# Kernel optimization log

Hardware: AMD Instinct MI355X
Metric: run time of the kernel (lower is better)

## Reference

```python
import jax, jax.numpy as jnp
from jax import lax
import numpy as np

T, B, INPUT_SIZE, HIDDEN, LAYERS, OUT_DIM = 256, 1000, 300, 2, 2, 1


def setup_inputs() -> dict:
    key = jax.random.key(0)
    ks = jax.random.split(key, 12)
    H4 = 4 * HIDDEN
    s = 0.1
    return {
        "x": jax.random.normal(ks[0], (T, B, INPUT_SIZE), dtype=jnp.float32),
        "h0": jnp.zeros((LAYERS, B, HIDDEN), dtype=jnp.float32),
        "c0": jnp.zeros((LAYERS, B, HIDDEN), dtype=jnp.float32),
        "W_ih0": jax.random.normal(ks[1], (H4, INPUT_SIZE), dtype=jnp.float32) * s,
        "W_hh0": jax.random.normal(ks[2], (H4, HIDDEN), dtype=jnp.float32) * s,
        "b_ih0": jax.random.normal(ks[3], (H4,), dtype=jnp.float32) * s,
        "b_hh0": jax.random.normal(ks[4], (H4,), dtype=jnp.float32) * s,
        "W_ih1": jax.random.normal(ks[5], (H4, HIDDEN), dtype=jnp.float32) * s,
        "W_hh1": jax.random.normal(ks[6], (H4, HIDDEN), dtype=jnp.float32) * s,
        "b_ih1": jax.random.normal(ks[7], (H4,), dtype=jnp.float32) * s,
        "b_hh1": jax.random.normal(ks[8], (H4,), dtype=jnp.float32) * s,
        "W_lin": jax.random.normal(ks[9], (OUT_DIM, HIDDEN), dtype=jnp.float32) * s,
        "b_lin": jax.random.normal(ks[10], (OUT_DIM,), dtype=jnp.float32) * s,
    }


def _lstm_layer(x, h0, c0, W_ih, W_hh, b_ih, b_hh):
    # x: [T, B, D_in]; PyTorch gate order i, f, g, o.
    # Precompute input projections for all timesteps at once (one big GEMM).
    xg = jnp.einsum('tbd,gd->tbg', x, W_ih) + (b_ih + b_hh)  # [T, B, 4H]

    def step(carry, xt):
        h, c = carry
        gates = xt + h @ W_hh.T  # [B, 4H]
        i, f, g, o = jnp.split(gates, 4, axis=-1)
        c = jax.nn.sigmoid(f) * c + jax.nn.sigmoid(i) * jnp.tanh(g)
        h = jax.nn.sigmoid(o) * jnp.tanh(c)
        return (h, c), h

    (_, _), ys = lax.scan(step, (h0, c0), xg)
    return ys  # [T, B, H]


def reference(x, h0, c0, W_ih0, W_hh0, b_ih0, b_hh0, W_ih1, W_hh1, b_ih1, b_hh1, W_lin, b_lin):
    y0 = _lstm_layer(x, h0[0], c0[0], W_ih0, W_hh0, b_ih0, b_hh0)   # [T, B, H]
    y1 = _lstm_layer(y0, h0[1], c0[1], W_ih1, W_hh1, b_ih1, b_hh1)  # [T, B, H]
    pred = y1[-1] @ W_lin.T + b_lin  # [B, 1]
    return pred.reshape(-1)          # [B]
```

## Files before the change

kernel.cpp:

```cpp
#include <hip/hip_runtime.h>

#define T_STEPS 256
#define BATCH   1000
#define D_IN    300
#define H4      8
#define ROWS    32
#define TILE_F4 2400
#define NT      8
#define NBLK    1000

#define L2E   1.4426950408889634f
#define L2E2  2.8853900817779268f

__device__ __forceinline__ float fexp2(float x) {
#if __has_builtin(__builtin_amdgcn_exp2f)
    return __builtin_amdgcn_exp2f(x);
#else
    return exp2f(x);
#endif
}
__device__ __forceinline__ float sig2(float x) {
    return __builtin_amdgcn_rcpf(1.0f + fexp2(-x));
}
__device__ __forceinline__ float tanh2(float x) {
    return fmaf(-2.0f, __builtin_amdgcn_rcpf(1.0f + fexp2(x)), 1.0f);
}

__device__ __forceinline__ void gload16(const float4* g, float4* l) {
    __builtin_amdgcn_global_load_lds(
        (const __attribute__((address_space(1))) void*)g,
        (__attribute__((address_space(3))) void*)l, 16, 0, 0);
}

__global__ __launch_bounds__(256) void xproj_kernel(
    const float* __restrict__ x, const float* __restrict__ W,
    const float* __restrict__ b_ih, const float* __restrict__ b_hh,
    float* __restrict__ xg)
{
    __shared__ __align__(16) float xs[2][2560 * 4];
    __shared__ __align__(16) float ws[768 * 4];

    const int tid   = threadIdx.x;
    const int wbase = tid & ~63;

    const float4* xf4 = (const float4*)x;
    const float4* wf4 = (const float4*)W;
    float4* xs0 = (float4*)xs[0];
    float4* xs1 = (float4*)xs[1];
    float4* wsf = (float4*)ws;

    const long tile0 = (long)blockIdx.x * NT;

    const int g = tid & 7;
    const int r = tid >> 3;
    const float bias  = b_ih[g] + b_hh[g];
    const float scale = (g == 4 || g == 5) ? L2E2 : L2E;

#pragma unroll
    for (int j = 0; j < 3; ++j) {
        int k  = j * 256 + tid;
        int gk = k < 600 ? k : 599;
        gload16(wf4 + gk, wsf + (j * 256 + wbase));
    }
#pragma unroll
    for (int j = 0; j < 10; ++j) {
        int k  = j * 256 + tid;
        int gk = k < TILE_F4 ? k : TILE_F4 - 1;
        gload16(xf4 + tile0 * TILE_F4 + gk, xs0 + (j * 256 + wbase));
    }
    asm volatile("s_waitcnt vmcnt(0)" ::: "memory");
    __builtin_amdgcn_s_barrier();

    const float4* wr = wsf + g * 75;

    for (int i = 0; i < NT; ++i) {
        if (i + 1 < NT) {
            float4* nbuf = (i & 1) ? xs0 : xs1;
            long tb = (tile0 + i + 1) * TILE_F4;
#pragma unroll
            for (int j = 0; j < 10; ++j) {
                int k  = j * 256 + tid;
                int gk = k < TILE_F4 ? k : TILE_F4 - 1;
                gload16(xf4 + tb + gk, nbuf + (j * 256 + wbase));
            }
        }

        const float4* xr = ((i & 1) ? xs1 : xs0) + r * 75;
        float a0 = 0.f, a1 = 0.f, a2 = 0.f, a3 = 0.f;
#pragma unroll 5
        for (int k = 0; k < 75; ++k) {
            float4 xv = xr[k];
            float4 wv = wr[k];
            a0 += xv.x * wv.x; a1 += xv.y * wv.y;
            a2 += xv.z * wv.z; a3 += xv.w * wv.w;
        }
        xg[(tile0 + i) * 256 + tid] = ((a0 + a1) + (a2 + a3) + bias) * scale;

        if (i + 1 < NT) {
            asm volatile("s_waitcnt vmcnt(1)" ::: "memory");
            __builtin_amdgcn_s_barrier();
        }
    }
}

__global__ __launch_bounds__(64) void lstm_seq_kernel(
    const float* __restrict__ xg,
    const float* __restrict__ h0in, const float* __restrict__ c0in,
    const float* __restrict__ Whh0, const float* __restrict__ Wih1,
    const float* __restrict__ Whh1, const float* __restrict__ bih1,
    const float* __restrict__ bhh1, const float* __restrict__ Wlin,
    const float* __restrict__ blin, float* __restrict__ out)
{
    int b = blockIdx.x * 64 + threadIdx.x;
    bool active = (b < BATCH);
    int bb = active ? b : (BATCH - 1);

    float whh0[H4][2], wih1[H4][2], whh1[H4][2], bias1[H4];
#pragma unroll
    for (int k = 0; k < H4; ++k) {
        float f = (k == 4 || k == 5) ? L2E2 : L2E;
        whh0[k][0] = Whh0[2 * k] * f; whh0[k][1] = Whh0[2 * k + 1] * f;
        wih1[k][0] = Wih1[2 * k] * f; wih1[k][1] = Wih1[2 * k + 1] * f;
        whh1[k][0] = Whh1[2 * k] * f; whh1[k][1] = Whh1[2 * k + 1] * f;
        bias1[k]   = (bih1[k] + bhh1[k]) * f;
    }

    float h0a = h0in[2 * bb],             h0b = h0in[2 * bb + 1];
    float c0a = c0in[2 * bb],             c0b = c0in[2 * bb + 1];
    float h1a = h0in[2 * BATCH + 2 * bb], h1b = h0in[2 * BATCH + 2 * bb + 1];
    float c1a = c0in[2 * BATCH + 2 * bb], c1b = c0in[2 * BATCH + 2 * bb + 1];

    const float4* __restrict__ xp = (const float4*)xg;

    float4 plo[4], phi[4];
#pragma unroll
    for (int t = 0; t < 4; ++t) {
        plo[t] = xp[(t * BATCH + bb) * 2];
        phi[t] = xp[(t * BATCH + bb) * 2 + 1];
    }

    float p[H4];
#pragma unroll
    for (int k = 0; k < H4; ++k)
        p[k] = bias1[k] + h1a * whh1[k][0] + h1b * whh1[k][1];

#pragma unroll 4
    for (int t = 0; t < T_STEPS; ++t) {
        int s = t & 3;
        float4 l4 = plo[s], h4 = phi[s];
        if (t + 4 < T_STEPS) {
            plo[s] = xp[((t + 4) * BATCH + bb) * 2];
            phi[s] = xp[((t + 4) * BATCH + bb) * 2 + 1];
        }
        float xv[H4] = {l4.x, l4.y, l4.z, l4.w, h4.x, h4.y, h4.z, h4.w};

        float gt[H4];
#pragma unroll
        for (int k = 0; k < H4; ++k)
            gt[k] = xv[k] + h0a * whh0[k][0] + h0b * whh0[k][1];
        c0a = sig2(gt[2]) * c0a + sig2(gt[0]) * tanh2(gt[4]);
        c0b = sig2(gt[3]) * c0b + sig2(gt[1]) * tanh2(gt[5]);
        h0a = sig2(gt[6]) * tanh2(c0a * L2E2);
        h0b = sig2(gt[7]) * tanh2(c0b * L2E2);

        float qt[H4];
#pragma unroll
        for (int k = 0; k < H4; ++k)
            qt[k] = p[k] + h0a * wih1[k][0] + h0b * wih1[k][1];
        c1a = sig2(qt[2]) * c1a + sig2(qt[0]) * tanh2(qt[4]);
        c1b = sig2(qt[3]) * c1b + sig2(qt[1]) * tanh2(qt[5]);
        h1a = sig2(qt[6]) * tanh2(c1a * L2E2);
        h1b = sig2(qt[7]) * tanh2(c1b * L2E2);

#pragma unroll
        for (int k = 0; k < H4; ++k)
            p[k] = bias1[k] + h1a * whh1[k][0] + h1b * whh1[k][1];
    }

    if (active)
        out[b] = h1a * Wlin[0] + h1b * Wlin[1] + blin[0];
}

extern "C" void kernel_launch(void* const* d_in, const int* in_sizes, int n_in,
                              void* d_out, int out_size, void* d_ws, size_t ws_size,
                              hipStream_t stream) {
    const float* x      = (const float*)d_in[0];
    const float* h0     = (const float*)d_in[1];
    const float* c0     = (const float*)d_in[2];
    const float* W_ih0  = (const float*)d_in[3];
    const float* W_hh0  = (const float*)d_in[4];
    const float* b_ih0  = (const float*)d_in[5];
    const float* b_hh0  = (const float*)d_in[6];
    const float* W_ih1  = (const float*)d_in[7];
    const float* W_hh1  = (const float*)d_in[8];
    const float* b_ih1  = (const float*)d_in[9];
    const float* b_hh1  = (const float*)d_in[10];
    const float* W_lin  = (const float*)d_in[11];
    const float* b_lin  = (const float*)d_in[12];
    float* out = (float*)d_out;
    float* xg  = (float*)d_ws;

    xproj_kernel<<<NBLK, 256, 0, stream>>>(x, W_ih0, b_ih0, b_hh0, xg);
    lstm_seq_kernel<<<(BATCH + 63) / 64, 64, 0, stream>>>(
        xg, h0, c0, W_hh0, W_ih1, W_hh1, b_ih1, b_hh1, W_lin, b_lin, out);
}
```

Before: 588.5 us.

## Rewrite input projection to stream x directly with quad-lane split-K dot products

The input-projection kernel drops the double-buffered LDS staging of x tiles through global_load_lds. Instead, each group of four lanes reads two rows of x straight from global memory, splits the 300-wide dot product across the lanes, and computes all 8 gates per row with weights kept in LDS. Partial sums are combined with xor shuffles and written out as float2. This removes the LDS round-trip and barriers for x and doubles the block count. In exchange it depends on direct global loads being coalesced enough and raises register pressure from 16 accumulators per thread.

```diff
diff --git a/kernel.cpp b/kernel.cpp
--- a/kernel.cpp
+++ b/kernel.cpp
@@ -4,10 +4,9 @@
 #define BATCH   1000
 #define D_IN    300
 #define H4      8
-#define ROWS    32
-#define TILE_F4 2400
-#define NT      8
-#define NBLK    1000
+#define NF4     75
+#define RPB     128
+#define NBLK    2000
 
 #define L2E   1.4426950408889634f
 #define L2E2  2.8853900817779268f
@@ -26,10 +25,8 @@
     return fmaf(-2.0f, __builtin_amdgcn_rcpf(1.0f + fexp2(x)), 1.0f);
 }
 
-__device__ __forceinline__ void gload16(const float4* g, float4* l) {
-    __builtin_amdgcn_global_load_lds(
-        (const __attribute__((address_space(1))) void*)g,
-        (__attribute__((address_space(3))) void*)l, 16, 0, 0);
+__device__ __forceinline__ float dot4acc(float4 a, float4 b, float acc) {
+    return fmaf(a.x, b.x, fmaf(a.y, b.y, fmaf(a.z, b.z, fmaf(a.w, b.w, acc))));
 }
 
 __global__ __launch_bounds__(256) void xproj_kernel(
@@ -37,70 +34,69 @@
     const float* __restrict__ b_ih, const float* __restrict__ b_hh,
     float* __restrict__ xg)
 {
-    __shared__ __align__(16) float xs[2][2560 * 4];
-    __shared__ __align__(16) float ws[768 * 4];
-
-    const int tid   = threadIdx.x;
-    const int wbase = tid & ~63;
-
-    const float4* xf4 = (const float4*)x;
-    const float4* wf4 = (const float4*)W;
-    float4* xs0 = (float4*)xs[0];
-    float4* xs1 = (float4*)xs[1];
-    float4* wsf = (float4*)ws;
-
-    const long tile0 = (long)blockIdx.x * NT;
-
-    const int g = tid & 7;
-    const int r = tid >> 3;
-    const float bias  = b_ih[g] + b_hh[g];
-    const float scale = (g == 4 || g == 5) ? L2E2 : L2E;
-
-#pragma unroll
-    for (int j = 0; j < 3; ++j) {
-        int k  = j * 256 + tid;
-        int gk = k < 600 ? k : 599;
-        gload16(wf4 + gk, wsf + (j * 256 + wbase));
-    }
-#pragma unroll
-    for (int j = 0; j < 10; ++j) {
-        int k  = j * 256 + tid;
-        int gk = k < TILE_F4 ? k : TILE_F4 - 1;
-        gload16(xf4 + tile0 * TILE_F4 + gk, xs0 + (j * 256 + wbase));
-    }
-    asm volatile("s_waitcnt vmcnt(0)" ::: "memory");
-    __builtin_amdgcn_s_barrier();
-
-    const float4* wr = wsf + g * 75;
-
-    for (int i = 0; i < NT; ++i) {
-        if (i + 1 < NT) {
-            float4* nbuf = (i & 1) ? xs0 : xs1;
-            long tb = (tile0 + i + 1) * TILE_F4;
-#pragma unroll
-            for (int j = 0; j < 10; ++j) {
-                int k  = j * 256 + tid;
-                int gk = k < TILE_F4 ? k : TILE_F4 - 1;
-                gload16(xf4 + tb + gk, nbuf + (j * 256 + wbase));
+    __shared__ __align__(16) float4 ws4[H4 * NF4];
+
+    const int tid = threadIdx.x;
+    const float4* __restrict__ w4 = (const float4*)W;
+    for (int k = tid; k < H4 * NF4; k += 256)
+        ws4[k] = w4[k];
+    __syncthreads();
+
+    const int  lane = tid & 3;
+    const int  quad = tid >> 2;
+    const long row0 = (long)blockIdx.x * RPB + (long)quad * 2;
+
+    const float4* __restrict__ x0 = (const float4*)x + row0 * NF4;
+    const float4* __restrict__ x1 = x0 + NF4;
+
+    float acc0[H4], acc1[H4];
+#pragma unroll
+    for (int g = 0; g < H4; ++g) { acc0[g] = 0.f; acc1[g] = 0.f; }
+
+#pragma unroll 3
+    for (int i = 0; i < 18; ++i) {
+        const int k = 4 * i + lane;
+        float4 xa = x0[k];
+        float4 xb = x1[k];
+#pragma unroll
+        for (int g = 0; g < H4; ++g) {
+            float4 wv = ws4[g * NF4 + k];
+            acc0[g] = dot4acc(xa, wv, acc0[g]);
+            acc1[g] = dot4acc(xb, wv, acc1[g]);
+        }
+    }
+    {
+        const int k = 72 + lane;
+        if (k < NF4) {
+            float4 xa = x0[k];
+            float4 xb = x1[k];
+#pragma unroll
+            for (int g = 0; g < H4; ++g) {
+                float4 wv = ws4[g * NF4 + k];
+                acc0[g] = dot4acc(xa, wv, acc0[g]);
+                acc1[g] = dot4acc(xb, wv, acc1[g]);
             }
         }
-
-        const float4* xr = ((i & 1) ? xs1 : xs0) + r * 75;
-        float a0 = 0.f, a1 = 0.f, a2 = 0.f, a3 = 0.f;
-#pragma unroll 5
-        for (int k = 0; k < 75; ++k) {
-            float4 xv = xr[k];
-            float4 wv = wr[k];
-            a0 += xv.x * wv.x; a1 += xv.y * wv.y;
-            a2 += xv.z * wv.z; a3 += xv.w * wv.w;
-        }
-        xg[(tile0 + i) * 256 + tid] = ((a0 + a1) + (a2 + a3) + bias) * scale;
-
-        if (i + 1 < NT) {
-            asm volatile("s_waitcnt vmcnt(1)" ::: "memory");
-            __builtin_amdgcn_s_barrier();
-        }
-    }
+    }
+
+#pragma unroll
+    for (int g = 0; g < H4; ++g) {
+        acc0[g] += __shfl_xor(acc0[g], 1);
+        acc0[g] += __shfl_xor(acc0[g], 2);
+        acc1[g] += __shfl_xor(acc1[g], 1);
+        acc1[g] += __shfl_xor(acc1[g], 2);
+    }
+
+    const int   g0 = lane * 2;
+    const float b0 = b_ih[g0]     + b_hh[g0];
+    const float b1 = b_ih[g0 + 1] + b_hh[g0 + 1];
+    const float sc = (lane == 2) ? L2E2 : L2E;
+
+    float2* __restrict__ out2 = (float2*)xg;
+    float2 o0 = { (acc0[g0] + b0) * sc, (acc0[g0 + 1] + b1) * sc };
+    float2 o1 = { (acc1[g0] + b0) * sc, (acc1[g0 + 1] + b1) * sc };
+    out2[row0 * 4 + lane]       = o0;
+    out2[(row0 + 1) * 4 + lane] = o1;
 }
 
 __global__ __launch_bounds__(64) void lstm_seq_kernel(
```

Result: faster. 555.8 us (-5.6%).
